# Performance work log

Hardware: AMD Instinct MI355X
Metric: run time of the kernel (lower is better)

## Reference

```python
import jax, jax.numpy as jnp
import numpy as np

EPS = 1e-5  # GroupNorm eps


def setup_inputs() -> dict:
    key = jax.random.key(0)
    ks = jax.random.split(key, 12)
    D, H, I = 512, 8, 64
    B, L = 2, 1024
    g = 0.01  # xavier gain used in reset_parameters
    inp = {
        "x": jax.random.normal(ks[0], (B, L, D), jnp.float32),
        "w_z": jax.random.normal(ks[1], (D, D), jnp.float32) * g,
        "b_z": jnp.zeros((D,), jnp.float32),
        "w_za": jax.random.normal(ks[2], (D, D), jnp.float32) * g,
        "b_za": jnp.zeros((D,), jnp.float32),
        "w_ang": jax.random.normal(ks[3], (D, H), jnp.float32) * g,
        "b_ang": jnp.zeros((H,), jnp.float32),
        "w_abs": jax.random.normal(ks[4], (D, H), jnp.float32) * g,
        "b_abs": jnp.zeros((H,), jnp.float32),
        "w_y": jax.random.normal(ks[5], (D, D), jnp.float32) * g,
        "b_y": jnp.zeros((D,), jnp.float32),
        "w_ya": jax.random.normal(ks[6], (D, D), jnp.float32) * g,
        "b_ya": jnp.zeros((D,), jnp.float32),
        "gn_w": jnp.ones((H,), jnp.float32),
        "gn_b": jnp.zeros((H,), jnp.float32),
        "lc_r": jax.random.normal(ks[7], (H, I), jnp.float32),
        "lc_i": jax.random.normal(ks[8], (H, I), jnp.float32),
    }
    return inp


def reference(x, w_z, b_z, w_za, b_za, w_ang, b_ang, w_abs, b_abs,
              w_y, b_y, w_ya, b_ya, gn_w, gn_b, lc_r, lc_i):
    B, L, D = x.shape
    H = gn_w.shape[0]
    I = D // H
    silu = jax.nn.silu
    xf = x.astype(jnp.float32)

    # gated value, promoted to complex:  [B, L, H, I]
    z = ((xf @ w_z + b_z) * silu(xf @ w_za + b_za)).astype(jnp.complex64).reshape(B, L, H, I)

    # per-head log-decay phazor: [B, L, H] complex
    scale = (0.001 ** jnp.linspace(0.0, 1.0, H)).astype(jnp.float32)
    ln_ph = (silu(xf @ w_ang + b_ang) * 1j - jax.nn.sigmoid(xf @ w_abs + b_abs)) * scale

    # FFT of ones => circular conv with ones = cumulative sum along axis 1
    ones_fft = jnp.fft.fft(jnp.ones((L,), jnp.float32), n=2 * L)

    # ln_phazor repeated over m then tril(-1) over the LAST TWO dims (m, h),
    # exactly matching torch.Tensor.tril semantics on a 'b l m h' tensor.
    masked = jnp.tril(jnp.broadcast_to(ln_ph[:, :, None, :], (B, L, L, H)), -1)
    mfft = jnp.fft.fft(masked, n=2 * L, axis=1)
    mconv = jnp.fft.ifft(mfft * ones_fft[None, :, None, None], axis=1)[:, :L]
    ph_masked = jnp.tril(jnp.exp(mconv))  # tril over (m, h)

    h_inner = jnp.einsum('blmh,bmhi->blhi', ph_masked, z)

    pfft = jnp.fft.fft(ln_ph, n=2 * L, axis=1)
    pconv = jnp.fft.ifft(pfft * ones_fft[None, :, None], axis=1)[:, :L]
    last_conv = lc_r + 1j * lc_i  # [H, I] complex (last_conv_init broadcast over batch)
    h_cross = jnp.exp(pconv)[..., None] * last_conv[None, None]  # [B, L, H, I]

    h = (h_inner + h_cross).real  # [B, L, H, I]

    # GroupNorm(H groups, H channels) on (B*L, H, I): per-(sample, head) norm over I
    mean = h.mean(axis=-1, keepdims=True)
    var = h.var(axis=-1, keepdims=True)
    hn = (h - mean) / jnp.sqrt(var + EPS) * gn_w[:, None] + gn_b[:, None]
    h_norm = hn.reshape(B, L, D)

    y = (h_norm @ w_y + b_y) * silu(xf @ w_ya + b_ya)
    return y.astype(x.dtype)
```

## Files before the change

kernel.cpp:

```cpp
#include <hip/hip_runtime.h>
#include <math.h>

#define D_ 512
#define H_ 8
#define I_ 64
#define L_ 1024

typedef __attribute__((ext_vector_type(8))) short short8;
typedef __attribute__((ext_vector_type(4))) float f32x4;

__device__ __forceinline__ float sigmoidf_(float x) { return 1.f / (1.f + expf(-x)); }
__device__ __forceinline__ float siluf_(float x) { return x / (1.f + expf(-x)); }

__device__ __forceinline__ unsigned short f2bf(float f) {
    unsigned u = __float_as_uint(f);
    u += 0x7fffu + ((u >> 16) & 1u);
    return (unsigned short)(u >> 16);
}
__device__ __forceinline__ float bf2f(unsigned short v) {
    return __uint_as_float((unsigned)v << 16);
}

#define RS 80
#define RSS 40

__global__ __launch_bounds__(256) void k1_prep(
    const float* __restrict__ x,
    const float* __restrict__ w0, const float* __restrict__ w1,
    const float* __restrict__ w2, const float* __restrict__ w3,
    unsigned short* __restrict__ t0, unsigned short* __restrict__ t1,
    unsigned short* __restrict__ t2, unsigned short* __restrict__ t3,
    const float* __restrict__ w_ang, const float* __restrict__ b_ang,
    const float* __restrict__ w_abs, const float* __restrict__ b_abs,
    float* __restrict__ a_out, float* __restrict__ r_out)
{
    __shared__ float sm[64][65];
    const int tid = threadIdx.x;
    const int bid = blockIdx.x;
    if (bid < 256) {
        int zsel = bid >> 6, tile = bid & 63;
        const float* src = zsel == 0 ? w0 : zsel == 1 ? w1 : zsel == 2 ? w2 : w3;
        unsigned short* dst = zsel == 0 ? t0 : zsel == 1 ? t1 : zsel == 2 ? t2 : t3;
        const int k0 = (tile >> 3) * 64, n0 = (tile & 7) * 64;
#pragma unroll
        for (int i = 0; i < 16; ++i) {
            int idx = tid + i * 256;
            int rr = idx >> 6, cc = idx & 63;
            sm[rr][cc] = src[(size_t)(k0 + rr) * 512 + n0 + cc];
        }
        __syncthreads();
#pragma unroll
        for (int i = 0; i < 16; ++i) {
            int idx = tid + i * 256;
            int rr = idx >> 6, cc = idx & 63;
            dst[(size_t)(n0 + rr) * 512 + k0 + cc] = f2bf(sm[cc][rr]);
        }
        return;
    }
    {
        int t = bid - 256;
        const int s = tid & 3, c = (tid >> 2) & 15, r = tid >> 6;
        const int n = t * 4 + r;
        const int h = c & 7;
        const float* wp = (c < 8) ? w_ang : w_abs;
        const float* xr = x + (size_t)n * D_;
        float acc = 0.f;
#pragma unroll 4
        for (int i = 0; i < 128; ++i) {
            int k = i * 4 + s;
            acc = fmaf(xr[k], wp[k * H_ + h], acc);
        }
        acc += __shfl_xor(acc, 1);
        acc += __shfl_xor(acc, 2);
        if (s == 0) {
            const float scale = expf(-6.9077552789821368f * (h * (1.0f / 7.0f)));
            if (c < 8) { float p = acc + b_ang[h]; a_out[(size_t)n * H_ + h] = siluf_(p) * scale; }
            else       { float p = acc + b_abs[h]; r_out[(size_t)n * H_ + h] = sigmoidf_(p) * scale; }
        }
    }
}

__global__ __launch_bounds__(256) void k2_gemm3_scan(
    const float* __restrict__ x,
    const unsigned short* __restrict__ Wz, const unsigned short* __restrict__ Wza,
    const unsigned short* __restrict__ Wya,
    const float* __restrict__ b_z, const float* __restrict__ b_za, const float* __restrict__ b_ya,
    unsigned short* __restrict__ gateb, float* __restrict__ Zs_part, float* __restrict__ zdiag,
    const float* __restrict__ a_arr, const float* __restrict__ r_arr,
    float* __restrict__ Si, float* __restrict__ Sr)
{
    __shared__ short As[2][64 * RSS];
    __shared__ short Bs[2][3][64 * RSS];
    __shared__ float red[64][8];
    __shared__ float2 buf[2][256];
    const int tid = threadIdx.x;
    const int bid = blockIdx.x;

    if (bid < 16) {
        const int b = bid >> 3, h = bid & 7;
        float2 v[4];
        float2 run = make_float2(0.f, 0.f);
        const size_t base = ((size_t)b * L_ + tid * 4) * H_ + h;
#pragma unroll
        for (int j = 0; j < 4; ++j) {
            run.x += a_arr[base + j * H_];
            run.y += r_arr[base + j * H_];
            v[j] = run;
        }
        buf[0][tid] = run;
        __syncthreads();
        int src = 0;
        for (int off = 1; off < 256; off <<= 1) {
            float2 val = buf[src][tid];
            if (tid >= off) { float2 q = buf[src][tid - off]; val.x += q.x; val.y += q.y; }
            buf[src ^ 1][tid] = val;
            src ^= 1;
            __syncthreads();
        }
        float2 excl = make_float2(0.f, 0.f);
        if (tid > 0) excl = buf[src][tid - 1];
#pragma unroll
        for (int j = 0; j < 4; ++j) {
            Si[base + j * H_] = v[j].x + excl.x;
            Sr[base + j * H_] = -(v[j].y + excl.y);
        }
        return;
    }

    const int u = bid - 16;
    const int rblk = (u & 7) * 4 + (u >> 6);
    const int bx = (u >> 3) & 7;
    const int lane = tid & 63, w = tid >> 6;
    const int wm = w >> 1, wn = w & 1;
    const int row0 = rblk * 64, col0 = bx * 64;

    const f32x4 zf = {0.f, 0.f, 0.f, 0.f};
    f32x4 accz[2][2], accza[2][2], accya[2][2];
#pragma unroll
    for (int a = 0; a < 2; ++a)
#pragma unroll
        for (int bq = 0; bq < 2; ++bq) { accz[a][bq] = zf; accza[a][bq] = zf; accya[a][bq] = zf; }

    const int sr_ = tid >> 2, sc_ = tid & 3;
    const int sld = sr_ * RS + sc_ * 16;
    const float* gAx = x + (size_t)(row0 + sr_) * 512 + sc_ * 8;
    const unsigned short* gWz  = Wz  + (size_t)(col0 + sr_) * 512 + sc_ * 8;
    const unsigned short* gWza = Wza + (size_t)(col0 + sr_) * 512 + sc_ * 8;
    const unsigned short* gWya = Wya + (size_t)(col0 + sr_) * 512 + sc_ * 8;

    float4 ra0, ra1; int4 rz, rza, rya;
#define K2_LOAD(K) { ra0 = *(const float4*)(gAx + (K)); ra1 = *(const float4*)(gAx + (K) + 4); \
                     rz  = *(const int4*)(gWz  + (K)); rza = *(const int4*)(gWza + (K)); \
                     rya = *(const int4*)(gWya + (K)); }
#define K2_WRITE(BUF) { short8 ab; \
                        ab[0]=(short)f2bf(ra0.x); ab[1]=(short)f2bf(ra0.y); \
                        ab[2]=(short)f2bf(ra0.z); ab[3]=(short)f2bf(ra0.w); \
                        ab[4]=(short)f2bf(ra1.x); ab[5]=(short)f2bf(ra1.y); \
                        ab[6]=(short)f2bf(ra1.z); ab[7]=(short)f2bf(ra1.w); \
                        *(short8*)((char*)As[BUF] + sld) = ab; \
                        *(int4*)((char*)Bs[BUF][0] + sld) = rz; \
                        *(int4*)((char*)Bs[BUF][1] + sld) = rza; \
                        *(int4*)((char*)Bs[BUF][2] + sld) = rya; }

    K2_LOAD(0);
    K2_WRITE(0);
    K2_LOAD(32);
    __syncthreads();

    int cur = 0;
    for (int s = 0; s < 16; ++s) {
        if (s < 15) {
            K2_WRITE(cur ^ 1);
            if (s < 14) K2_LOAD((s + 2) * 32);
        }
        short8 af[2], bz[2], bza[2], bya[2];
        const int ck = (lane >> 4) << 4;
#pragma unroll
        for (int fi = 0; fi < 2; ++fi) {
            int rr = wm * 32 + fi * 16 + (lane & 15);
            af[fi] = *(const short8*)((const char*)As[cur] + rr * RS + ck);
        }
#pragma unroll
        for (int fj = 0; fj < 2; ++fj) {
            int rr = wn * 32 + fj * 16 + (lane & 15);
            bz[fj]  = *(const short8*)((const char*)Bs[cur][0] + rr * RS + ck);
            bza[fj] = *(const short8*)((const char*)Bs[cur][1] + rr * RS + ck);
            bya[fj] = *(const short8*)((const char*)Bs[cur][2] + rr * RS + ck);
        }
#pragma unroll
        for (int fi = 0; fi < 2; ++fi)
#pragma unroll
            for (int fj = 0; fj < 2; ++fj) {
                accz[fi][fj]  = __builtin_amdgcn_mfma_f32_16x16x32_bf16(af[fi], bz[fj],  accz[fi][fj],  0, 0, 0);
                accza[fi][fj] = __builtin_amdgcn_mfma_f32_16x16x32_bf16(af[fi], bza[fj], accza[fi][fj], 0, 0, 0);
                accya[fi][fj] = __builtin_amdgcn_mfma_f32_16x16x32_bf16(af[fi], bya[fj], accya[fi][fj], 0, 0, 0);
            }
        __syncthreads();
        cur ^= 1;
    }
#undef K2_LOAD
#undef K2_WRITE

    const bool first = (rblk & 15) == 0;
    const int b8 = (rblk >> 4) * 8;
#pragma unroll
    for (int fj = 0; fj < 2; ++fj) {
        float lsum = 0.f;
        int lc = wn * 32 + fj * 16 + (lane & 15);
        int col = col0 + lc;
        float Bz = b_z[col], Bza = b_za[col], Bya = b_ya[col];
#pragma unroll
        for (int fi = 0; fi < 2; ++fi) {
#pragma unroll
            for (int q = 0; q < 4; ++q) {
                int lr = wm * 32 + fi * 16 + ((lane >> 4) << 2) + q;
                int row = row0 + lr;
                float pz = accz[fi][fj][q] + Bz;
                float pza = accza[fi][fj][q] + Bza;
                float v = pz * siluf_(pza);
                gateb[(size_t)row * 512 + col] = f2bf(siluf_(accya[fi][fj][q] + Bya));
                if (!first || lr > bx) lsum += v;
                if (first && lr == bx) zdiag[(b8 + bx) * 64 + lc] = v;
            }
        }
        red[lc][wm * 4 + (lane >> 4)] = lsum;
    }
    __syncthreads();
    if (tid < 64) {
        float s = 0.f;
#pragma unroll
        for (int j = 0; j < 8; ++j) s += red[tid][j];
        Zs_part[((size_t)rblk * 8 + bx) * 64 + tid] = s;
    }
}

__global__ __launch_bounds__(512) void k3_hgn_gemm_y(
    const unsigned short* __restrict__ Wy, const float* __restrict__ b_y,
    const unsigned short* __restrict__ gateb,
    const float* __restrict__ Sr, const float* __restrict__ Si,
    const float* __restrict__ Zs_part, const float* __restrict__ zdiag,
    const float* __restrict__ lc_r, const float* __restrict__ lc_i,
    const float* __restrict__ gn_w, const float* __restrict__ gn_b,
    float* __restrict__ y)
{
    __shared__ unsigned short hA[64][520];
    __shared__ short Bs[2][64 * RSS];
    __shared__ float Cr[8][65], Ci[8][65], Zd[8][65];
    const int tid = threadIdx.x;
    const int lane = tid & 63, w = tid >> 6;
    const int cbx = blockIdx.x & 7;
    const int rpair = blockIdx.x >> 3;
    const int row0 = rpair * 64, col0 = cbx * 64;
    const int b = row0 >> 10;

    const int brow = tid >> 3, bsc = tid & 7;
    const size_t gB = (size_t)(col0 + brow) * 512 + bsc * 4;
    const int bwr = brow * RS + bsc * 8;
    int2 rw0 = *(const int2*)(Wy + gB);
    int2 rw1 = *(const int2*)(Wy + gB + 32);

    {
        int h = tid >> 6, i = tid & 63;
        float s = 0.f;
#pragma unroll
        for (int rb = 0; rb < 16; ++rb)
            s += Zs_part[(((size_t)b * 16 + rb) * 8 + h) * 64 + i];
        Cr[h][i] = s + lc_r[h * 64 + i];
        Ci[h][i] = lc_i[h * 64 + i];
        Zd[h][i] = zdiag[((size_t)b * 8 + h) * 64 + i];
    }
    __syncthreads();

    {
        const int r = tid >> 3, h = tid & 7;
        const int row = row0 + r;
        const float sr = Sr[(size_t)row * 8 + h];
        const float si = Si[(size_t)row * 8 + h];
        const float er = expf(sr);
        const float ca = er * cosf(si), sb = er * sinf(si);
        float sum = 0.f, sq = 0.f;
#pragma unroll 8
        for (int i = 0; i < 64; ++i) {
            float hv = Zd[h][i] + ca * Cr[h][i] - sb * Ci[h][i];
            sum += hv; sq += hv * hv;
        }
        const float mean = sum * (1.f / 64.f);
        const float inv = rsqrtf(sq * (1.f / 64.f) - mean * mean + 1e-5f);
        const float gw = gn_w[h] * inv;
        const float gb = gn_b[h] - mean * gw;
#pragma unroll
        for (int s8 = 0; s8 < 8; ++s8) {
            short8 pk;
#pragma unroll
            for (int j = 0; j < 8; ++j) {
                int i = s8 * 8 + j;
                float hv = Zd[h][i] + ca * Cr[h][i] - sb * Ci[h][i];
                pk[j] = (short)f2bf(hv * gw + gb);
            }
            int slot = (s8 + h) & 7;
            *(short8*)((char*)&hA[r][0] + h * 128 + slot * 16) = pk;
        }
    }
    *(int2*)((char*)Bs[0] + bwr) = rw0;
    __syncthreads();

    const int wm = w >> 2, wn = w & 3;
    const f32x4 zf = {0.f, 0.f, 0.f, 0.f};
    f32x4 acc[2] = {zf, zf};

    int cur = 0;
    for (int s = 0; s < 16; ++s) {
        if (s < 15) {
            *(int2*)((char*)Bs[cur ^ 1] + bwr) = rw1;
            if (s < 14) rw1 = *(const int2*)(Wy + gB + (s + 2) * 32);
        }
        const int k0 = s * 32;
        short8 af[2], bf;
        const int hk = k0 >> 6;
        const int t = ((k0 & 32) >> 3) + (lane >> 4);
        const int slot = (t + hk) & 7;
#pragma unroll
        for (int fi = 0; fi < 2; ++fi) {
            int rr = wm * 32 + fi * 16 + (lane & 15);
            af[fi] = *(const short8*)((const char*)&hA[rr][0] + hk * 128 + slot * 16);
        }
        {
            int rr = wn * 16 + (lane & 15);
            bf = *(const short8*)((const char*)Bs[cur] + rr * RS + ((lane >> 4) << 4));
        }
        acc[0] = __builtin_amdgcn_mfma_f32_16x16x32_bf16(af[0], bf, acc[0], 0, 0, 0);
        acc[1] = __builtin_amdgcn_mfma_f32_16x16x32_bf16(af[1], bf, acc[1], 0, 0, 0);
        __syncthreads();
        cur ^= 1;
    }

    const int col = col0 + wn * 16 + (lane & 15);
    const float By = b_y[col];
#pragma unroll
    for (int fi = 0; fi < 2; ++fi)
#pragma unroll
        for (int q = 0; q < 4; ++q) {
            int row = row0 + wm * 32 + fi * 16 + ((lane >> 4) << 2) + q;
            size_t idx = (size_t)row * 512 + col;
            y[idx] = (acc[fi][q] + By) * bf2f(gateb[idx]);
        }
}

extern "C" void kernel_launch(void* const* d_in, const int* in_sizes, int n_in,
                              void* d_out, int out_size, void* d_ws, size_t ws_size,
                              hipStream_t stream) {
    (void)n_in; (void)out_size; (void)ws_size;
    const float* x     = (const float*)d_in[0];
    const float* w_z   = (const float*)d_in[1];
    const float* b_z   = (const float*)d_in[2];
    const float* w_za  = (const float*)d_in[3];
    const float* b_za  = (const float*)d_in[4];
    const float* w_ang = (const float*)d_in[5];
    const float* b_ang = (const float*)d_in[6];
    const float* w_abs = (const float*)d_in[7];
    const float* b_abs = (const float*)d_in[8];
    const float* w_y   = (const float*)d_in[9];
    const float* b_y   = (const float*)d_in[10];
    const float* w_ya  = (const float*)d_in[11];
    const float* b_ya  = (const float*)d_in[12];
    const float* gn_w  = (const float*)d_in[13];
    const float* gn_b  = (const float*)d_in[14];
    const float* lc_r  = (const float*)d_in[15];
    const float* lc_i  = (const float*)d_in[16];
    float* y = (float*)d_out;

    const int BL = in_sizes[0] / D_;
    const int B  = BL / L_;

    unsigned short* wtz  = (unsigned short*)d_ws;
    unsigned short* wtza = wtz  + 512 * 512;
    unsigned short* wtya = wtza + 512 * 512;
    unsigned short* wty  = wtya + 512 * 512;
    unsigned short* gateb= wty  + 512 * 512;
    float* a_arr = (float*)(gateb + (size_t)BL * 512);
    float* r_arr = a_arr + (size_t)BL * H_;
    float* Si    = r_arr + (size_t)BL * H_;
    float* Sr    = Si    + (size_t)BL * H_;
    float* zdiag = Sr    + (size_t)BL * H_;
    float* Zs_part = zdiag + (size_t)B * H_ * I_;

    k1_prep<<<256 + BL / 4, 256, 0, stream>>>(
        x, w_z, w_za, w_ya, w_y, wtz, wtza, wtya, wty,
        w_ang, b_ang, w_abs, b_abs, a_arr, r_arr);
    k2_gemm3_scan<<<16 + (BL / 64) * 8, 256, 0, stream>>>(
        x, wtz, wtza, wtya, b_z, b_za, b_ya,
        gateb, Zs_part, zdiag, a_arr, r_arr, Si, Sr);
    k3_hgn_gemm_y<<<(BL / 64) * 8, 512, 0, stream>>>(
        wty, b_y, gateb, Sr, Si, Zs_part, zdiag, lc_r, lc_i, gn_w, gn_b, y);
}
```

Baseline: 44.24 us.

## Split fused three-GEMM kernel into separate z/za and ya block groups

The k2 kernel previously had each block compute all three projections (z, za, ya) for one 64x64 tile. Now the grid is doubled: one set of blocks computes the z/za pair and the Zs partial sums, and a second set computes only the ya gate. This doubles the block count (256 to 512 GEMM blocks), uses more CUs and lowers per-block LDS and register pressure. The cost is that the x tile is loaded and converted to bf16 twice, and the two block kinds do unequal amounts of work. The hardcoded 272 offset assumes BL=2048.

```diff
diff --git a/kernel.cpp b/kernel.cpp
--- a/kernel.cpp
+++ b/kernel.cpp
@@ -80,7 +80,7 @@
     }
 }
 
-__global__ __launch_bounds__(256) void k2_gemm3_scan(
+__global__ __launch_bounds__(256) void k2_split(
     const float* __restrict__ x,
     const unsigned short* __restrict__ Wz, const unsigned short* __restrict__ Wza,
     const unsigned short* __restrict__ Wya,
@@ -90,7 +90,7 @@
     float* __restrict__ Si, float* __restrict__ Sr)
 {
     __shared__ short As[2][64 * RSS];
-    __shared__ short Bs[2][3][64 * RSS];
+    __shared__ short Bs[2][2][64 * RSS];
     __shared__ float red[64][8];
     __shared__ float2 buf[2][256];
     const int tid = threadIdx.x;
@@ -127,7 +127,8 @@
         return;
     }
 
-    const int u = bid - 16;
+    const bool zza = bid < 272;
+    const int u = zza ? (bid - 16) : (bid - 272);
     const int rblk = (u & 7) * 4 + (u >> 6);
     const int bx = (u >> 3) & 7;
     const int lane = tid & 63, w = tid >> 6;
@@ -135,102 +136,163 @@
     const int row0 = rblk * 64, col0 = bx * 64;
 
     const f32x4 zf = {0.f, 0.f, 0.f, 0.f};
-    f32x4 accz[2][2], accza[2][2], accya[2][2];
-#pragma unroll
-    for (int a = 0; a < 2; ++a)
-#pragma unroll
-        for (int bq = 0; bq < 2; ++bq) { accz[a][bq] = zf; accza[a][bq] = zf; accya[a][bq] = zf; }
-
     const int sr_ = tid >> 2, sc_ = tid & 3;
     const int sld = sr_ * RS + sc_ * 16;
     const float* gAx = x + (size_t)(row0 + sr_) * 512 + sc_ * 8;
-    const unsigned short* gWz  = Wz  + (size_t)(col0 + sr_) * 512 + sc_ * 8;
-    const unsigned short* gWza = Wza + (size_t)(col0 + sr_) * 512 + sc_ * 8;
-    const unsigned short* gWya = Wya + (size_t)(col0 + sr_) * 512 + sc_ * 8;
-
-    float4 ra0, ra1; int4 rz, rza, rya;
-#define K2_LOAD(K) { ra0 = *(const float4*)(gAx + (K)); ra1 = *(const float4*)(gAx + (K) + 4); \
-                     rz  = *(const int4*)(gWz  + (K)); rza = *(const int4*)(gWza + (K)); \
-                     rya = *(const int4*)(gWya + (K)); }
-#define K2_WRITE(BUF) { short8 ab; \
-                        ab[0]=(short)f2bf(ra0.x); ab[1]=(short)f2bf(ra0.y); \
-                        ab[2]=(short)f2bf(ra0.z); ab[3]=(short)f2bf(ra0.w); \
-                        ab[4]=(short)f2bf(ra1.x); ab[5]=(short)f2bf(ra1.y); \
-                        ab[6]=(short)f2bf(ra1.z); ab[7]=(short)f2bf(ra1.w); \
-                        *(short8*)((char*)As[BUF] + sld) = ab; \
-                        *(int4*)((char*)Bs[BUF][0] + sld) = rz; \
-                        *(int4*)((char*)Bs[BUF][1] + sld) = rza; \
-                        *(int4*)((char*)Bs[BUF][2] + sld) = rya; }
-
-    K2_LOAD(0);
-    K2_WRITE(0);
-    K2_LOAD(32);
-    __syncthreads();
-
-    int cur = 0;
-    for (int s = 0; s < 16; ++s) {
-        if (s < 15) {
-            K2_WRITE(cur ^ 1);
-            if (s < 14) K2_LOAD((s + 2) * 32);
-        }
-        short8 af[2], bz[2], bza[2], bya[2];
-        const int ck = (lane >> 4) << 4;
-#pragma unroll
-        for (int fi = 0; fi < 2; ++fi) {
-            int rr = wm * 32 + fi * 16 + (lane & 15);
-            af[fi] = *(const short8*)((const char*)As[cur] + rr * RS + ck);
-        }
+    const int ck = (lane >> 4) << 4;
+
+    if (zza) {
+        const unsigned short* gWz  = Wz  + (size_t)(col0 + sr_) * 512 + sc_ * 8;
+        const unsigned short* gWza = Wza + (size_t)(col0 + sr_) * 512 + sc_ * 8;
+        f32x4 accz[2][2], accza[2][2];
+#pragma unroll
+        for (int a = 0; a < 2; ++a)
+#pragma unroll
+            for (int bq = 0; bq < 2; ++bq) { accz[a][bq] = zf; accza[a][bq] = zf; }
+
+        float4 ra0, ra1; int4 rz, rza;
+#define Z_LOAD(K) { ra0 = *(const float4*)(gAx + (K)); ra1 = *(const float4*)(gAx + (K) + 4); \
+                    rz  = *(const int4*)(gWz  + (K)); rza = *(const int4*)(gWza + (K)); }
+#define Z_WRITE(BUF) { short8 ab; \
+                       ab[0]=(short)f2bf(ra0.x); ab[1]=(short)f2bf(ra0.y); \
+                       ab[2]=(short)f2bf(ra0.z); ab[3]=(short)f2bf(ra0.w); \
+                       ab[4]=(short)f2bf(ra1.x); ab[5]=(short)f2bf(ra1.y); \
+                       ab[6]=(short)f2bf(ra1.z); ab[7]=(short)f2bf(ra1.w); \
+                       *(short8*)((char*)As[BUF] + sld) = ab; \
+                       *(int4*)((char*)Bs[BUF][0] + sld) = rz; \
+                       *(int4*)((char*)Bs[BUF][1] + sld) = rza; }
+
+        Z_LOAD(0);
+        Z_WRITE(0);
+        Z_LOAD(32);
+        __syncthreads();
+
+        int cur = 0;
+        for (int s = 0; s < 16; ++s) {
+            if (s < 15) {
+                Z_WRITE(cur ^ 1);
+                if (s < 14) Z_LOAD((s + 2) * 32);
+            }
+            short8 af[2], bz[2], bza[2];
+#pragma unroll
+            for (int fi = 0; fi < 2; ++fi) {
+                int rr = wm * 32 + fi * 16 + (lane & 15);
+                af[fi] = *(const short8*)((const char*)As[cur] + rr * RS + ck);
+            }
+#pragma unroll
+            for (int fj = 0; fj < 2; ++fj) {
+                int rr = wn * 32 + fj * 16 + (lane & 15);
+                bz[fj]  = *(const short8*)((const char*)Bs[cur][0] + rr * RS + ck);
+                bza[fj] = *(const short8*)((const char*)Bs[cur][1] + rr * RS + ck);
+            }
+#pragma unroll
+            for (int fi = 0; fi < 2; ++fi)
+#pragma unroll
+                for (int fj = 0; fj < 2; ++fj) {
+                    accz[fi][fj]  = __builtin_amdgcn_mfma_f32_16x16x32_bf16(af[fi], bz[fj],  accz[fi][fj],  0, 0, 0);
+                    accza[fi][fj] = __builtin_amdgcn_mfma_f32_16x16x32_bf16(af[fi], bza[fj], accza[fi][fj], 0, 0, 0);
+                }
+            __syncthreads();
+            cur ^= 1;
+        }
+#undef Z_LOAD
+#undef Z_WRITE
+
+        const bool first = (rblk & 15) == 0;
+        const int b8 = (rblk >> 4) * 8;
 #pragma unroll
         for (int fj = 0; fj < 2; ++fj) {
-            int rr = wn * 32 + fj * 16 + (lane & 15);
-            bz[fj]  = *(const short8*)((const char*)Bs[cur][0] + rr * RS + ck);
-            bza[fj] = *(const short8*)((const char*)Bs[cur][1] + rr * RS + ck);
-            bya[fj] = *(const short8*)((const char*)Bs[cur][2] + rr * RS + ck);
-        }
-#pragma unroll
-        for (int fi = 0; fi < 2; ++fi)
+            float lsum = 0.f;
+            int lc = wn * 32 + fj * 16 + (lane & 15);
+            int col = col0 + lc;
+            float Bz = b_z[col], Bza = b_za[col];
+#pragma unroll
+            for (int fi = 0; fi < 2; ++fi) {
+#pragma unroll
+                for (int q = 0; q < 4; ++q) {
+                    int lr = wm * 32 + fi * 16 + ((lane >> 4) << 2) + q;
+                    float pz = accz[fi][fj][q] + Bz;
+                    float pza = accza[fi][fj][q] + Bza;
+                    float v = pz * siluf_(pza);
+                    if (!first || lr > bx) lsum += v;
+                    if (first && lr == bx) zdiag[(b8 + bx) * 64 + lc] = v;
+                }
+            }
+            red[lc][wm * 4 + (lane >> 4)] = lsum;
+        }
+        __syncthreads();
+        if (tid < 64) {
+            float s = 0.f;
+#pragma unroll
+            for (int j = 0; j < 8; ++j) s += red[tid][j];
+            Zs_part[((size_t)rblk * 8 + bx) * 64 + tid] = s;
+        }
+    } else {
+        const unsigned short* gWya = Wya + (size_t)(col0 + sr_) * 512 + sc_ * 8;
+        f32x4 accya[2][2];
+#pragma unroll
+        for (int a = 0; a < 2; ++a)
+#pragma unroll
+            for (int bq = 0; bq < 2; ++bq) accya[a][bq] = zf;
+
+        float4 ra0, ra1; int4 rya;
+#define Y_LOAD(K) { ra0 = *(const float4*)(gAx + (K)); ra1 = *(const float4*)(gAx + (K) + 4); \
+                    rya = *(const int4*)(gWya + (K)); }
+#define Y_WRITE(BUF) { short8 ab; \
+                       ab[0]=(short)f2bf(ra0.x); ab[1]=(short)f2bf(ra0.y); \
+                       ab[2]=(short)f2bf(ra0.z); ab[3]=(short)f2bf(ra0.w); \
+                       ab[4]=(short)f2bf(ra1.x); ab[5]=(short)f2bf(ra1.y); \
+                       ab[6]=(short)f2bf(ra1.z); ab[7]=(short)f2bf(ra1.w); \
+                       *(short8*)((char*)As[BUF] + sld) = ab; \
+                       *(int4*)((char*)Bs[BUF][0] + sld) = rya; }
+
+        Y_LOAD(0);
+        Y_WRITE(0);
+        Y_LOAD(32);
+        __syncthreads();
+
+        int cur = 0;
+        for (int s = 0; s < 16; ++s) {
+            if (s < 15) {
+                Y_WRITE(cur ^ 1);
+                if (s < 14) Y_LOAD((s + 2) * 32);
+            }
+            short8 af[2], bya[2];
+#pragma unroll
+            for (int fi = 0; fi < 2; ++fi) {
+                int rr = wm * 32 + fi * 16 + (lane & 15);
+                af[fi] = *(const short8*)((const char*)As[cur] + rr * RS + ck);
+            }
 #pragma unroll
             for (int fj = 0; fj < 2; ++fj) {
-                accz[fi][fj]  = __builtin_amdgcn_mfma_f32_16x16x32_bf16(af[fi], bz[fj],  accz[fi][fj],  0, 0, 0);
-                accza[fi][fj] = __builtin_amdgcn_mfma_f32_16x16x32_bf16(af[fi], bza[fj], accza[fi][fj], 0, 0, 0);
-                accya[fi][fj] = __builtin_amdgcn_mfma_f32_16x16x32_bf16(af[fi], bya[fj], accya[fi][fj], 0, 0, 0);
-            }
-        __syncthreads();
-        cur ^= 1;
-    }
-#undef K2_LOAD
-#undef K2_WRITE
-
-    const bool first = (rblk & 15) == 0;
-    const int b8 = (rblk >> 4) * 8;
-#pragma unroll
-    for (int fj = 0; fj < 2; ++fj) {
-        float lsum = 0.f;
-        int lc = wn * 32 + fj * 16 + (lane & 15);
-        int col = col0 + lc;
-        float Bz = b_z[col], Bza = b_za[col], Bya = b_ya[col];
-#pragma unroll
-        for (int fi = 0; fi < 2; ++fi) {
-#pragma unroll
-            for (int q = 0; q < 4; ++q) {
-                int lr = wm * 32 + fi * 16 + ((lane >> 4) << 2) + q;
-                int row = row0 + lr;
-                float pz = accz[fi][fj][q] + Bz;
-                float pza = accza[fi][fj][q] + Bza;
-                float v = pz * siluf_(pza);
-                gateb[(size_t)row * 512 + col] = f2bf(siluf_(accya[fi][fj][q] + Bya));
-                if (!first || lr > bx) lsum += v;
-                if (first && lr == bx) zdiag[(b8 + bx) * 64 + lc] = v;
-            }
-        }
-        red[lc][wm * 4 + (lane >> 4)] = lsum;
-    }
-    __syncthreads();
-    if (tid < 64) {
-        float s = 0.f;
-#pragma unroll
-        for (int j = 0; j < 8; ++j) s += red[tid][j];
-        Zs_part[((size_t)rblk * 8 + bx) * 64 + tid] = s;
+                int rr = wn * 32 + fj * 16 + (lane & 15);
+                bya[fj] = *(const short8*)((const char*)Bs[cur][0] + rr * RS + ck);
+            }
+#pragma unroll
+            for (int fi = 0; fi < 2; ++fi)
+#pragma unroll
+                for (int fj = 0; fj < 2; ++fj)
+                    accya[fi][fj] = __builtin_amdgcn_mfma_f32_16x16x32_bf16(af[fi], bya[fj], accya[fi][fj], 0, 0, 0);
+            __syncthreads();
+            cur ^= 1;
+        }
+#undef Y_LOAD
+#undef Y_WRITE
+
+#pragma unroll
+        for (int fj = 0; fj < 2; ++fj) {
+            int lc = wn * 32 + fj * 16 + (lane & 15);
+            int col = col0 + lc;
+            float Bya = b_ya[col];
+#pragma unroll
+            for (int fi = 0; fi < 2; ++fi)
+#pragma unroll
+                for (int q = 0; q < 4; ++q) {
+                    int lr = wm * 32 + fi * 16 + ((lane >> 4) << 2) + q;
+                    int row = row0 + lr;
+                    gateb[(size_t)row * 512 + col] = f2bf(siluf_(accya[fi][fj][q] + Bya));
+                }
+        }
     }
 }
 
@@ -384,12 +446,14 @@
     float* zdiag = Sr    + (size_t)BL * H_;
     float* Zs_part = zdiag + (size_t)B * H_ * I_;
 
+    const int ntiles = (BL / 64) * 8;
+
     k1_prep<<<256 + BL / 4, 256, 0, stream>>>(
         x, w_z, w_za, w_ya, w_y, wtz, wtza, wtya, wty,
         w_ang, b_ang, w_abs, b_abs, a_arr, r_arr);
-    k2_gemm3_scan<<<16 + (BL / 64) * 8, 256, 0, stream>>>(
+    k2_split<<<16 + 2 * ntiles, 256, 0, stream>>>(
         x, wtz, wtza, wtya, b_z, b_za, b_ya,
         gateb, Zs_part, zdiag, a_arr, r_arr, Si, Sr);
-    k3_hgn_gemm_y<<<(BL / 64) * 8, 512, 0, stream>>>(
+    k3_hgn_gemm_y<<<ntiles, 512, 0, stream>>>(
         wty, b_y, gateb, Sr, Si, Zs_part, zdiag, lc_r, lc_i, gn_w, gn_b, y);
 }
```

Result: faster. 40.48 us (-8.5%).
